# Optimization experiments

Hardware: AMD Instinct MI355X
Metric: run time of the kernel (lower is better)

The kernel has to match this reference:

```python
import jax, jax.numpy as jnp
import numpy as np


def setup_inputs() -> dict:
    key = jax.random.key(0)
    feature = jax.random.normal(key, (32, 64, 128, 128), dtype=jnp.float32)
    return {"feature": feature}


def reference(feature):
    # feature: [B, C, H, W]
    B, C, H, W = feature.shape
    mgr = feature.mean()  # global mean over all elements

    # Per-(sample, channel) argmax location; row-major first-occurrence matches
    # the original strict '>' scan.
    flat_idx = jnp.argmax(feature.reshape(B, C, H * W), axis=-1)  # [B, C]
    max_x = flat_idx // W  # row index
    max_y = flat_idx % W   # col index

    i = jnp.arange(H)
    j = jnp.arange(W)
    # squared distance from each pixel to its channel's argmax: [B, C, H, W]
    dist2 = ((max_x[:, :, None, None] - i[None, None, :, None]) ** 2
             + (max_y[:, :, None, None] - j[None, None, None, :]) ** 2)
    dist2 = dist2.astype(feature.dtype)

    f2 = feature * feature
    dis_loss = jnp.sum(f2 * dist2)

    # max over OTHER channels at each pixel: top-2 over channel axis,
    # use 2nd max only for the channel that is the (first) argmax.
    t = jnp.moveaxis(feature, 1, -1)  # [B, H, W, C]
    top2, _ = jax.lax.top_k(t, 2)    # [B, H, W, 2]
    m1 = top2[..., 0][:, None, :, :]  # [B, 1, H, W]
    m2 = top2[..., 1][:, None, :, :]
    amax_c = jnp.argmax(t, axis=-1)[:, None, :, :]  # [B, 1, H, W]
    c_ids = jnp.arange(C)[None, :, None, None]      # [1, C, 1, 1]
    max_others = jnp.where(c_ids == amax_c, m2, m1)  # [B, C, H, W]

    div_loss = jnp.sum(f2 * (max_others - mgr) ** 2)

    n = B * C * H * W
    return dis_loss / n, div_loss / n
```

## Files before the change

kernel.cpp:

```cpp
#include <hip/hip_runtime.h>

#define HW     16384
#define WDIM   128
#define CDIM   64
#define BDIM   32
#define NBF    4096
#define NBC    2048

#define OFF_WMAX  0
#define OFF_WIDX  (1u << 20)
#define OFF_WSF   (2u << 20)
#define OFF_WS0   (3u << 20)
#define OFF_WSJ   (4u << 20)
#define OFF_WSQJ  (5u << 20)
#define OFF_WA1   (6u << 20)
#define OFF_WA2   ((6u << 20) + 32768u)
#define OFF_K3    ((6u << 20) + 65536u)

__global__ __launch_bounds__(256, 4) void f_fused(const float* __restrict__ feat,
                                                  float* __restrict__ wmax, int* __restrict__ widx,
                                                  float* __restrict__ wsf,  float* __restrict__ ws0,
                                                  float* __restrict__ wsj,  float* __restrict__ wsqj,
                                                  double* __restrict__ wa1, double* __restrict__ wa2) {
    __shared__ float tile[CDIM * 129];
    __shared__ float scratch[1792];
    __shared__ float sred[4];

    const int t  = threadIdx.x;
    const int bf = blockIdx.x;
    const int b  = bf >> 7, row = bf & 127;
    const float* src = feat + (size_t)b * CDIM * HW + (size_t)row * WDIM;

    float4 buf[8];
    #pragma unroll
    for (int k = 0; k < 8; ++k) {
        int idx = k * 256 + t;
        int c = idx >> 5, g = idx & 31;
        buf[k] = *(const float4*)(src + (size_t)c * HW + g * 4);
    }
    #pragma unroll
    for (int k = 0; k < 8; ++k) {
        int idx = k * 256 + t;
        int c = idx >> 5, g = idx & 31;
        float* dst = &tile[c * 129 + g * 4];
        dst[0] = buf[k].x; dst[1] = buf[k].y; dst[2] = buf[k].z; dst[3] = buf[k].w;
    }
    __syncthreads();

    const int px = t & 127, half = t >> 7;
    float m1 = -INFINITY, m2 = -INFINITY, s2 = 0.f;
    #pragma unroll
    for (int cc = 0; cc < 32; ++cc) {
        float x = tile[(half * 32 + cc) * 129 + px];
        if (x > m1) { m2 = m1; m1 = x; } else { m2 = fmaxf(m2, x); }
        s2 = fmaf(x, x, s2);
    }
    if (half) { scratch[px * 3] = m1; scratch[px * 3 + 1] = m2; scratch[px * 3 + 2] = s2; }
    __syncthreads();

    const int ch = t & 63, sub = t >> 6, p0 = sub * 32;
    float bm = -INFINITY; int bi = 0;
    float sf = 0.f, s0 = 0.f, sjl = 0.f, sql = 0.f;
    #pragma unroll
    for (int i = 0; i < 32; ++i) {
        float x = tile[ch * 129 + p0 + i];
        if (x > bm) { bm = x; bi = i; }
        sf += x;
        float q = x * x;
        s0 += q;
        sjl = fmaf(q, (float)i, sjl);
        sql = fmaf(q, (float)(i * i), sql);
    }

    if (!half) {
        float n1 = scratch[px * 3], n2 = scratch[px * 3 + 1], s2b = scratch[px * 3 + 2];
        float mm1 = fmaxf(m1, n1);
        float mm2 = fmaxf(fminf(m1, n1), fmaxf(m2, n2));
        float S2 = s2 + s2b;
        float qq = mm1 * mm1, rr = S2 - qq;
        float a1 = qq * rr + mm2 * mm2 * qq;
        float a2 = mm1 * rr + mm2 * qq;
        #pragma unroll
        for (int off = 32; off > 0; off >>= 1) {
            a1 += __shfl_down(a1, off);
            a2 += __shfl_down(a2, off);
        }
        if (t == 0)  { sred[0] = a1; sred[1] = a2; }
        if (t == 64) { sred[2] = a1; sred[3] = a2; }
    }
    __syncthreads();

    {
        float sj  = fmaf((float)p0, s0, sjl);
        float sqj = fmaf((float)(p0 * p0), s0, fmaf(2.f * (float)p0, sjl, sql));
        int o = (sub * 64 + ch) * 7;
        scratch[o]     = bm;
        scratch[o + 1] = __int_as_float(p0 + bi);
        scratch[o + 2] = sf; scratch[o + 3] = s0;
        scratch[o + 4] = sj; scratch[o + 5] = sqj;
    }
    if (t == 255) {
        wa1[bf] = (double)(sred[0] + sred[2]);
        wa2[bf] = (double)(sred[1] + sred[3]);
    }
    __syncthreads();

    if (t < 64) {
        float M = -INFINITY; int P = 0;
        float SF = 0.f, S0 = 0.f, SJ = 0.f, SQ = 0.f;
        #pragma unroll
        for (int s = 0; s < 4; ++s) {
            int oo = (s * 64 + t) * 7;
            float m = scratch[oo];
            if (m > M) { M = m; P = __float_as_int(scratch[oo + 1]); }
            SF += scratch[oo + 2]; S0 += scratch[oo + 3];
            SJ += scratch[oo + 4]; SQ += scratch[oo + 5];
        }
        int out = t * 4096 + bf;
        wmax[out] = M; widx[out] = P;
        wsf[out] = SF; ws0[out] = S0; wsj[out] = SJ; wsqj[out] = SQ;
    }
}

__global__ __launch_bounds__(128) void k3_channel(const float* __restrict__ wmax, const int* __restrict__ widx,
                                                  const float* __restrict__ wsf,  const float* __restrict__ ws0,
                                                  const float* __restrict__ wsj,  const float* __restrict__ wsqj,
                                                  double* __restrict__ k3out) {
    const int bc = blockIdx.x;
    const int b = bc >> 6, c = bc & 63;
    const int t = threadIdx.x;
    const int idx = c * 4096 + b * 128 + t;

    float m = wmax[idx]; int px = widx[idx];
    float sf = wsf[idx], s0 = ws0[idx], sj = wsj[idx], sqj = wsqj[idx];

    __shared__ float rm[128]; __shared__ int rr[128]; __shared__ int rp[128];
    rm[t] = m; rr[t] = t; rp[t] = px;
    __syncthreads();
    for (int off = 64; off > 0; off >>= 1) {
        if (t < off) {
            float mo = rm[t + off];
            if (mo > rm[t] || (mo == rm[t] && rr[t + off] < rr[t])) {
                rm[t] = mo; rr[t] = rr[t + off]; rp[t] = rp[t + off];
            }
        }
        __syncthreads();
    }
    const int mi = rr[0], mj = rp[0];

    double di = (double)(mi - t);
    double disc = (di * di + (double)mj * (double)mj) * (double)s0
                - 2.0 * (double)mj * (double)sj + (double)sqj;

    __shared__ double rd[128], rsf[128], rs0[128];
    rd[t] = disc; rsf[t] = (double)sf; rs0[t] = (double)s0;
    __syncthreads();
    for (int off = 64; off > 0; off >>= 1) {
        if (t < off) { rd[t] += rd[t + off]; rsf[t] += rsf[t + off]; rs0[t] += rs0[t + off]; }
        __syncthreads();
    }
    if (t == 0) {
        k3out[bc * 3]     = rsf[0];
        k3out[bc * 3 + 1] = rs0[0];
        k3out[bc * 3 + 2] = rd[0];
    }
}

__global__ __launch_bounds__(256) void k4_final(const double* __restrict__ k3out,
                                                const double* __restrict__ wa1,
                                                const double* __restrict__ wa2,
                                                float* __restrict__ out) {
    const int t = threadIdx.x;
    double sf = 0, s0 = 0, dis = 0, a1 = 0, a2 = 0;
    for (int i = t; i < NBC; i += 256) {
        sf += k3out[i * 3]; s0 += k3out[i * 3 + 1]; dis += k3out[i * 3 + 2];
    }
    for (int i = t; i < NBF; i += 256) { a1 += wa1[i]; a2 += wa2[i]; }

    __shared__ double r[5][256];
    r[0][t] = sf; r[1][t] = s0; r[2][t] = dis; r[3][t] = a1; r[4][t] = a2;
    __syncthreads();
    for (int off = 128; off > 0; off >>= 1) {
        if (t < off) {
            #pragma unroll
            for (int q = 0; q < 5; ++q) r[q][t] += r[q][t + off];
        }
        __syncthreads();
    }
    if (t == 0) {
        const double n = 33554432.0;
        double mgr = r[0][0] / n;
        out[0] = (float)(r[2][0] / n);
        out[1] = (float)((r[3][0] - 2.0 * mgr * r[4][0] + mgr * mgr * r[1][0]) / n);
    }
}

extern "C" void kernel_launch(void* const* d_in, const int* in_sizes, int n_in,
                              void* d_out, int out_size, void* d_ws, size_t ws_size,
                              hipStream_t stream) {
    const float* feat = (const float*)d_in[0];
    float* out = (float*)d_out;
    char* ws = (char*)d_ws;

    float*  wmax = (float*)(ws + OFF_WMAX);
    int*    widx = (int*)  (ws + OFF_WIDX);
    float*  wsf  = (float*)(ws + OFF_WSF);
    float*  ws0  = (float*)(ws + OFF_WS0);
    float*  wsj  = (float*)(ws + OFF_WSJ);
    float*  wsqj = (float*)(ws + OFF_WSQJ);
    double* wa1  = (double*)(ws + OFF_WA1);
    double* wa2  = (double*)(ws + OFF_WA2);
    double* k3o  = (double*)(ws + OFF_K3);

    f_fused<<<NBF, 256, 0, stream>>>(feat, wmax, widx, wsf, ws0, wsj, wsqj, wa1, wa2);
    k3_channel<<<NBC, 128, 0, stream>>>(wmax, widx, wsf, ws0, wsj, wsqj, k3o);
    k4_final<<<1, 256, 0, stream>>>(k3o, wa1, wa2, out);
}
```

Before: 53.69 us.

## Process four rows per block with register prefetch of the next row

```diff
diff --git a/kernel.cpp b/kernel.cpp
--- a/kernel.cpp
+++ b/kernel.cpp
@@ -5,6 +5,7 @@
 #define CDIM   64
 #define BDIM   32
 #define NBF    4096
+#define NBG    1024
 #define NBC    2048
 
 #define OFF_WMAX  0
@@ -27,98 +28,121 @@
     __shared__ float sred[4];
 
     const int t  = threadIdx.x;
-    const int bf = blockIdx.x;
-    const int b  = bf >> 7, row = bf & 127;
-    const float* src = feat + (size_t)b * CDIM * HW + (size_t)row * WDIM;
+    const int bq = blockIdx.x;
+    const int b  = bq >> 5, rg = bq & 31;
+    const int row0 = rg * 4;
+    const float* srcb = feat + (size_t)b * CDIM * HW + (size_t)row0 * WDIM;
+
+    const int px = t & 127, half = t >> 7;
+    const int ch = t & 63, sub = t >> 6, p0 = sub * 32;
 
     float4 buf[8];
     #pragma unroll
     for (int k = 0; k < 8; ++k) {
         int idx = k * 256 + t;
         int c = idx >> 5, g = idx & 31;
-        buf[k] = *(const float4*)(src + (size_t)c * HW + g * 4);
-    }
+        buf[k] = *(const float4*)(srcb + (size_t)c * HW + g * 4);
+    }
+
     #pragma unroll
-    for (int k = 0; k < 8; ++k) {
-        int idx = k * 256 + t;
-        int c = idx >> 5, g = idx & 31;
-        float* dst = &tile[c * 129 + g * 4];
-        dst[0] = buf[k].x; dst[1] = buf[k].y; dst[2] = buf[k].z; dst[3] = buf[k].w;
-    }
-    __syncthreads();
-
-    const int px = t & 127, half = t >> 7;
-    float m1 = -INFINITY, m2 = -INFINITY, s2 = 0.f;
-    #pragma unroll
-    for (int cc = 0; cc < 32; ++cc) {
-        float x = tile[(half * 32 + cc) * 129 + px];
-        if (x > m1) { m2 = m1; m1 = x; } else { m2 = fmaxf(m2, x); }
-        s2 = fmaf(x, x, s2);
-    }
-    if (half) { scratch[px * 3] = m1; scratch[px * 3 + 1] = m2; scratch[px * 3 + 2] = s2; }
-    __syncthreads();
-
-    const int ch = t & 63, sub = t >> 6, p0 = sub * 32;
-    float bm = -INFINITY; int bi = 0;
-    float sf = 0.f, s0 = 0.f, sjl = 0.f, sql = 0.f;
-    #pragma unroll
-    for (int i = 0; i < 32; ++i) {
-        float x = tile[ch * 129 + p0 + i];
-        if (x > bm) { bm = x; bi = i; }
-        sf += x;
-        float q = x * x;
-        s0 += q;
-        sjl = fmaf(q, (float)i, sjl);
-        sql = fmaf(q, (float)(i * i), sql);
-    }
-
-    if (!half) {
-        float n1 = scratch[px * 3], n2 = scratch[px * 3 + 1], s2b = scratch[px * 3 + 2];
-        float mm1 = fmaxf(m1, n1);
-        float mm2 = fmaxf(fminf(m1, n1), fmaxf(m2, n2));
-        float S2 = s2 + s2b;
-        float qq = mm1 * mm1, rr = S2 - qq;
-        float a1 = qq * rr + mm2 * mm2 * qq;
-        float a2 = mm1 * rr + mm2 * qq;
+    for (int r = 0; r < 4; ++r) {
+        const int bf = b * 128 + row0 + r;
+
         #pragma unroll
-        for (int off = 32; off > 0; off >>= 1) {
-            a1 += __shfl_down(a1, off);
-            a2 += __shfl_down(a2, off);
-        }
-        if (t == 0)  { sred[0] = a1; sred[1] = a2; }
-        if (t == 64) { sred[2] = a1; sred[3] = a2; }
-    }
-    __syncthreads();
-
-    {
-        float sj  = fmaf((float)p0, s0, sjl);
-        float sqj = fmaf((float)(p0 * p0), s0, fmaf(2.f * (float)p0, sjl, sql));
-        int o = (sub * 64 + ch) * 7;
-        scratch[o]     = bm;
-        scratch[o + 1] = __int_as_float(p0 + bi);
-        scratch[o + 2] = sf; scratch[o + 3] = s0;
-        scratch[o + 4] = sj; scratch[o + 5] = sqj;
-    }
-    if (t == 255) {
-        wa1[bf] = (double)(sred[0] + sred[2]);
-        wa2[bf] = (double)(sred[1] + sred[3]);
-    }
-    __syncthreads();
-
-    if (t < 64) {
-        float M = -INFINITY; int P = 0;
-        float SF = 0.f, S0 = 0.f, SJ = 0.f, SQ = 0.f;
+        for (int k = 0; k < 8; ++k) {
+            int idx = k * 256 + t;
+            int c = idx >> 5, g = idx & 31;
+            float* dst = &tile[c * 129 + g * 4];
+            dst[0] = buf[k].x; dst[1] = buf[k].y; dst[2] = buf[k].z; dst[3] = buf[k].w;
+        }
+
+        float4 nbuf[8];
+        if (r < 3) {
+            #pragma unroll
+            for (int k = 0; k < 8; ++k) {
+                int idx = k * 256 + t;
+                int c = idx >> 5, g = idx & 31;
+                nbuf[k] = *(const float4*)(srcb + (size_t)(r + 1) * WDIM + (size_t)c * HW + g * 4);
+            }
+        }
+        __syncthreads();
+
+        float m1 = -INFINITY, m2 = -INFINITY, s2 = 0.f;
         #pragma unroll
-        for (int s = 0; s < 4; ++s) {
-            int oo = (s * 64 + t) * 7;
-            float m = scratch[oo];
-            if (m > M) { M = m; P = __float_as_int(scratch[oo + 1]); }
-            SF += scratch[oo + 2]; S0 += scratch[oo + 3];
-            SJ += scratch[oo + 4]; SQ += scratch[oo + 5];
-        }
-        int out = t * 4096 + bf;
-        wmax[out] = M; widx[out] = P;
-        wsf[out] = SF; ws0[out] = S0; wsj[out] = SJ; wsqj[out] = SQ;
+        for (int cc = 0; cc < 32; ++cc) {
+            float x = tile[(half * 32 + cc) * 129 + px];
+            if (x > m1) { m2 = m1; m1 = x; } else { m2 = fmaxf(m2, x); }
+            s2 = fmaf(x, x, s2);
+        }
+        if (half) { scratch[px * 3] = m1; scratch[px * 3 + 1] = m2; scratch[px * 3 + 2] = s2; }
+        __syncthreads();
+
+        float bm = -INFINITY; int bi = 0;
+        float sf = 0.f, s0 = 0.f, sjl = 0.f, sql = 0.f;
+        #pragma unroll
+        for (int i = 0; i < 32; ++i) {
+            float x = tile[ch * 129 + p0 + i];
+            if (x > bm) { bm = x; bi = i; }
+            sf += x;
+            float q = x * x;
+            s0 += q;
+            sjl = fmaf(q, (float)i, sjl);
+            sql = fmaf(q, (float)(i * i), sql);
+        }
+
+        if (!half) {
+            float n1 = scratch[px * 3], n2 = scratch[px * 3 + 1], s2b = scratch[px * 3 + 2];
+            float mm1 = fmaxf(m1, n1);
+            float mm2 = fmaxf(fminf(m1, n1), fmaxf(m2, n2));
+            float S2 = s2 + s2b;
+            float qq = mm1 * mm1, rr2 = S2 - qq;
+            float a1 = qq * rr2 + mm2 * mm2 * qq;
+            float a2 = mm1 * rr2 + mm2 * qq;
+            #pragma unroll
+            for (int off = 32; off > 0; off >>= 1) {
+                a1 += __shfl_down(a1, off);
+                a2 += __shfl_down(a2, off);
+            }
+            if (t == 0)  { sred[0] = a1; sred[1] = a2; }
+            if (t == 64) { sred[2] = a1; sred[3] = a2; }
+        }
+        __syncthreads();
+
+        {
+            float sj  = fmaf((float)p0, s0, sjl);
+            float sqj = fmaf((float)(p0 * p0), s0, fmaf(2.f * (float)p0, sjl, sql));
+            int o = (sub * 64 + ch) * 7;
+            scratch[o]     = bm;
+            scratch[o + 1] = __int_as_float(p0 + bi);
+            scratch[o + 2] = sf; scratch[o + 3] = s0;
+            scratch[o + 4] = sj; scratch[o + 5] = sqj;
+        }
+        if (t == 255) {
+            wa1[bf] = (double)(sred[0] + sred[2]);
+            wa2[bf] = (double)(sred[1] + sred[3]);
+        }
+        __syncthreads();
+
+        if (t < 64) {
+            float M = -INFINITY; int P = 0;
+            float SF = 0.f, S0 = 0.f, SJ = 0.f, SQ = 0.f;
+            #pragma unroll
+            for (int s = 0; s < 4; ++s) {
+                int oo = (s * 64 + t) * 7;
+                float m = scratch[oo];
+                if (m > M) { M = m; P = __float_as_int(scratch[oo + 1]); }
+                SF += scratch[oo + 2]; S0 += scratch[oo + 3];
+                SJ += scratch[oo + 4]; SQ += scratch[oo + 5];
+            }
+            int out = t * 4096 + bf;
+            wmax[out] = M; widx[out] = P;
+            wsf[out] = SF; ws0[out] = S0; wsj[out] = SJ; wsqj[out] = SQ;
+        }
+
+        if (r < 3) {
+            #pragma unroll
+            for (int k = 0; k < 8; ++k) buf[k] = nbuf[k];
+        }
     }
 }
 
@@ -212,7 +236,7 @@
     double* wa2  = (double*)(ws + OFF_WA2);
     double* k3o  = (double*)(ws + OFF_K3);
 
-    f_fused<<<NBF, 256, 0, stream>>>(feat, wmax, widx, wsf, ws0, wsj, wsqj, wa1, wa2);
+    f_fused<<<NBG, 256, 0, stream>>>(feat, wmax, widx, wsf, ws0, wsj, wsqj, wa1, wa2);
     k3_channel<<<NBC, 128, 0, stream>>>(wmax, widx, wsf, ws0, wsj, wsqj, k3o);
     k4_final<<<1, 256, 0, stream>>>(k3o, wa1, wa2, out);
 }
```

Result: slower. 61.91 us (+15.3%).

## Double-buffer row tiles with async global-to-LDS loads and XOR-swizzled layout

Applied to the files above, without the earlier changes.

```diff
diff --git a/kernel.cpp b/kernel.cpp
--- a/kernel.cpp
+++ b/kernel.cpp
@@ -1,9 +1,12 @@
 #include <hip/hip_runtime.h>
+#include <stdint.h>
 
 #define HW     16384
 #define WDIM   128
 #define CDIM   64
 #define BDIM   32
+#define ROWS   8
+#define NBG    512
 #define NBF    4096
 #define NBC    2048
 
@@ -17,108 +20,143 @@
 #define OFF_WA2   ((6u << 20) + 32768u)
 #define OFF_K3    ((6u << 20) + 65536u)
 
-__global__ __launch_bounds__(256, 4) void f_fused(const float* __restrict__ feat,
+__device__ __forceinline__ void dma16(const float* g, float* l) {
+    __builtin_amdgcn_global_load_lds(
+        (const __attribute__((address_space(1))) void*)g,
+        (__attribute__((address_space(3))) void*)l, 16, 0, 0);
+}
+
+#define BAR_LGKM() do { asm volatile("s_waitcnt lgkmcnt(0)" ::: "memory"); \
+                        __builtin_amdgcn_s_barrier(); } while (0)
+#define BAR_ALL()  do { asm volatile("s_waitcnt vmcnt(0) lgkmcnt(0)" ::: "memory"); \
+                        __builtin_amdgcn_s_barrier(); } while (0)
+
+__global__ __launch_bounds__(256, 2) void f_fused(const float* __restrict__ feat,
                                                   float* __restrict__ wmax, int* __restrict__ widx,
                                                   float* __restrict__ wsf,  float* __restrict__ ws0,
                                                   float* __restrict__ wsj,  float* __restrict__ wsqj,
                                                   double* __restrict__ wa1, double* __restrict__ wa2) {
-    __shared__ float tile[CDIM * 129];
+    __shared__ __align__(16) float tile[2][CDIM * 128];
     __shared__ float scratch[1792];
     __shared__ float sred[4];
 
     const int t  = threadIdx.x;
-    const int bf = blockIdx.x;
-    const int b  = bf >> 7, row = bf & 127;
-    const float* src = feat + (size_t)b * CDIM * HW + (size_t)row * WDIM;
-
-    float4 buf[8];
+    const int bq = blockIdx.x;
+    const int b  = bq >> 4, rg = bq & 15;
+    const int row0 = rg * ROWS;
+    const float* base = feat + (size_t)b * CDIM * HW + (size_t)row0 * WDIM;
+
+    int dma_c[8], dma_qx[8], dma_idx[8];
     #pragma unroll
     for (int k = 0; k < 8; ++k) {
         int idx = k * 256 + t;
-        int c = idx >> 5, g = idx & 31;
-        buf[k] = *(const float4*)(src + (size_t)c * HW + g * 4);
-    }
+        int c = idx >> 5, qp = idx & 31;
+        dma_idx[k] = idx; dma_c[k] = c; dma_qx[k] = qp ^ (c & 7);
+    }
+
+    const int px = t & 127, half = t >> 7;
+    const int pq = px >> 2, pm = px & 3;
+    const int ch = t & 63, sub = t >> 6, p0 = sub * 32;
+
     #pragma unroll
-    for (int k = 0; k < 8; ++k) {
-        int idx = k * 256 + t;
-        int c = idx >> 5, g = idx & 31;
-        float* dst = &tile[c * 129 + g * 4];
-        dst[0] = buf[k].x; dst[1] = buf[k].y; dst[2] = buf[k].z; dst[3] = buf[k].w;
-    }
-    __syncthreads();
-
-    const int px = t & 127, half = t >> 7;
-    float m1 = -INFINITY, m2 = -INFINITY, s2 = 0.f;
+    for (int k = 0; k < 8; ++k)
+        dma16(base + (size_t)dma_c[k] * HW + (dma_qx[k] << 2), &tile[0][dma_idx[k] * 4]);
+    BAR_ALL();
+
     #pragma unroll
-    for (int cc = 0; cc < 32; ++cc) {
-        float x = tile[(half * 32 + cc) * 129 + px];
-        if (x > m1) { m2 = m1; m1 = x; } else { m2 = fmaxf(m2, x); }
-        s2 = fmaf(x, x, s2);
-    }
-    if (half) { scratch[px * 3] = m1; scratch[px * 3 + 1] = m2; scratch[px * 3 + 2] = s2; }
-    __syncthreads();
-
-    const int ch = t & 63, sub = t >> 6, p0 = sub * 32;
-    float bm = -INFINITY; int bi = 0;
-    float sf = 0.f, s0 = 0.f, sjl = 0.f, sql = 0.f;
-    #pragma unroll
-    for (int i = 0; i < 32; ++i) {
-        float x = tile[ch * 129 + p0 + i];
-        if (x > bm) { bm = x; bi = i; }
-        sf += x;
-        float q = x * x;
-        s0 += q;
-        sjl = fmaf(q, (float)i, sjl);
-        sql = fmaf(q, (float)(i * i), sql);
-    }
-
-    if (!half) {
-        float n1 = scratch[px * 3], n2 = scratch[px * 3 + 1], s2b = scratch[px * 3 + 2];
-        float mm1 = fmaxf(m1, n1);
-        float mm2 = fmaxf(fminf(m1, n1), fmaxf(m2, n2));
-        float S2 = s2 + s2b;
-        float qq = mm1 * mm1, rr = S2 - qq;
-        float a1 = qq * rr + mm2 * mm2 * qq;
-        float a2 = mm1 * rr + mm2 * qq;
+    for (int r = 0; r < ROWS; ++r) {
+        const int cur = r & 1;
+        const int bf = b * 128 + row0 + r;
+
+        if (r < ROWS - 1) {
+            const float* nb = base + (size_t)(r + 1) * WDIM;
+            #pragma unroll
+            for (int k = 0; k < 8; ++k)
+                dma16(nb + (size_t)dma_c[k] * HW + (dma_qx[k] << 2), &tile[cur ^ 1][dma_idx[k] * 4]);
+        }
+
+        float m1 = -INFINITY, m2 = -INFINITY, s2 = 0.f;
         #pragma unroll
-        for (int off = 32; off > 0; off >>= 1) {
-            a1 += __shfl_down(a1, off);
-            a2 += __shfl_down(a2, off);
-        }
-        if (t == 0)  { sred[0] = a1; sred[1] = a2; }
-        if (t == 64) { sred[2] = a1; sred[3] = a2; }
-    }
-    __syncthreads();
-
-    {
-        float sj  = fmaf((float)p0, s0, sjl);
-        float sqj = fmaf((float)(p0 * p0), s0, fmaf(2.f * (float)p0, sjl, sql));
-        int o = (sub * 64 + ch) * 7;
-        scratch[o]     = bm;
-        scratch[o + 1] = __int_as_float(p0 + bi);
-        scratch[o + 2] = sf; scratch[o + 3] = s0;
-        scratch[o + 4] = sj; scratch[o + 5] = sqj;
-    }
-    if (t == 255) {
-        wa1[bf] = (double)(sred[0] + sred[2]);
-        wa2[bf] = (double)(sred[1] + sred[3]);
-    }
-    __syncthreads();
-
-    if (t < 64) {
-        float M = -INFINITY; int P = 0;
-        float SF = 0.f, S0 = 0.f, SJ = 0.f, SQ = 0.f;
+        for (int cc = 0; cc < 32; ++cc) {
+            int c = half * 32 + cc;
+            float x = tile[cur][c * 128 + ((pq ^ (c & 7)) << 2) + pm];
+            if (x > m1) { m2 = m1; m1 = x; } else { m2 = fmaxf(m2, x); }
+            s2 = fmaf(x, x, s2);
+        }
+        if (half) { scratch[px * 3] = m1; scratch[px * 3 + 1] = m2; scratch[px * 3 + 2] = s2; }
+        BAR_LGKM();
+
+        float bm = -INFINITY; int bi = 0;
+        float sf = 0.f, s0 = 0.f, sjl = 0.f, sql = 0.f;
         #pragma unroll
-        for (int s = 0; s < 4; ++s) {
-            int oo = (s * 64 + t) * 7;
-            float m = scratch[oo];
-            if (m > M) { M = m; P = __float_as_int(scratch[oo + 1]); }
-            SF += scratch[oo + 2]; S0 += scratch[oo + 3];
-            SJ += scratch[oo + 4]; SQ += scratch[oo + 5];
-        }
-        int out = t * 4096 + bf;
-        wmax[out] = M; widx[out] = P;
-        wsf[out] = SF; ws0[out] = S0; wsj[out] = SJ; wsqj[out] = SQ;
+        for (int qq = 0; qq < 8; ++qq) {
+            int qx = (p0 >> 2) + qq;
+            const float4 v = *reinterpret_cast<const float4*>(
+                &tile[cur][ch * 128 + ((qx ^ (ch & 7)) << 2)]);
+            float xs[4] = {v.x, v.y, v.z, v.w};
+            #pragma unroll
+            for (int e = 0; e < 4; ++e) {
+                int i = qq * 4 + e;
+                float x = xs[e];
+                if (x > bm) { bm = x; bi = i; }
+                sf += x;
+                float q = x * x;
+                s0 += q;
+                sjl = fmaf(q, (float)i, sjl);
+                sql = fmaf(q, (float)(i * i), sql);
+            }
+        }
+
+        if (!half) {
+            float n1 = scratch[px * 3], n2 = scratch[px * 3 + 1], s2b = scratch[px * 3 + 2];
+            float mm1 = fmaxf(m1, n1);
+            float mm2 = fmaxf(fminf(m1, n1), fmaxf(m2, n2));
+            float S2 = s2 + s2b;
+            float qq2 = mm1 * mm1, rr2 = S2 - qq2;
+            float a1 = qq2 * rr2 + mm2 * mm2 * qq2;
+            float a2 = mm1 * rr2 + mm2 * qq2;
+            #pragma unroll
+            for (int off = 32; off > 0; off >>= 1) {
+                a1 += __shfl_down(a1, off);
+                a2 += __shfl_down(a2, off);
+            }
+            if (t == 0)  { sred[0] = a1; sred[1] = a2; }
+            if (t == 64) { sred[2] = a1; sred[3] = a2; }
+        }
+        BAR_LGKM();
+
+        {
+            float sj  = fmaf((float)p0, s0, sjl);
+            float sqj = fmaf((float)(p0 * p0), s0, fmaf(2.f * (float)p0, sjl, sql));
+            int o = (sub * 64 + ch) * 7;
+            scratch[o]     = bm;
+            scratch[o + 1] = __int_as_float(p0 + bi);
+            scratch[o + 2] = sf; scratch[o + 3] = s0;
+            scratch[o + 4] = sj; scratch[o + 5] = sqj;
+        }
+        if (t == 255) {
+            wa1[bf] = (double)(sred[0] + sred[2]);
+            wa2[bf] = (double)(sred[1] + sred[3]);
+        }
+        BAR_LGKM();
+
+        if (t < 64) {
+            float M = -INFINITY; int P = 0;
+            float SF = 0.f, S0 = 0.f, SJ = 0.f, SQ = 0.f;
+            #pragma unroll
+            for (int s = 0; s < 4; ++s) {
+                int oo = (s * 64 + t) * 7;
+                float m = scratch[oo];
+                if (m > M) { M = m; P = __float_as_int(scratch[oo + 1]); }
+                SF += scratch[oo + 2]; S0 += scratch[oo + 3];
+                SJ += scratch[oo + 4]; SQ += scratch[oo + 5];
+            }
+            int out = t * 4096 + bf;
+            wmax[out] = M; widx[out] = P;
+            wsf[out] = SF; ws0[out] = S0; wsj[out] = SJ; wsqj[out] = SQ;
+        }
+
+        BAR_ALL();
     }
 }
 
@@ -212,7 +250,7 @@
     double* wa2  = (double*)(ws + OFF_WA2);
     double* k3o  = (double*)(ws + OFF_K3);
 
-    f_fused<<<NBF, 256, 0, stream>>>(feat, wmax, widx, wsf, ws0, wsj, wsqj, wa1, wa2);
+    f_fused<<<NBG, 256, 0, stream>>>(feat, wmax, widx, wsf, ws0, wsj, wsqj, wa1, wa2);
     k3_channel<<<NBC, 128, 0, stream>>>(wmax, widx, wsf, ws0, wsj, wsqj, k3o);
     k4_final<<<1, 256, 0, stream>>>(k3o, wa1, wa2, out);
 }
```

Result: slower. 59.12 us (+10.1%).
